# Kernel tuning notes

Hardware: AMD Instinct MI355X
Metric: run time of the kernel (lower is better)

Reference implementation:

```python
import jax, jax.numpy as jnp
import numpy as np

H = 8   # num_heads
K = 7   # kernel_size


def setup_inputs() -> dict:
    key = jax.random.key(0)
    k1, k2, k3 = jax.random.split(key, 3)
    T, B, C = 2048, 16, 512
    x = jax.random.normal(k1, (T, B, C), dtype=jnp.float32)
    query = jax.random.normal(k2, (T, B, C), dtype=jnp.float32)
    W = jax.random.normal(k3, (C, H * K), dtype=jnp.float32) * 0.02
    return {"x": x, "query": query, "W": W}


def reference(x, query, W):
    T, B, C = x.shape
    R = C // H
    # per-position, per-head kernel weights: Dense(H*K) on query, no bias
    weight = jnp.einsum('tbc,cn->tbn', query, W).reshape(T * B * H, K)
    weight = jax.nn.softmax(weight, axis=-1)  # weight_softmax=True; dropout rate 0 is identity
    # TF extract_patches with SAME padding along T: total pad K-1, more on the bottom
    pad_before = (K - 1) // 2
    pad_after = K - 1 - pad_before
    x_pad = jnp.pad(x, ((pad_before, pad_after), (0, 0), (0, 0)))
    idx = jnp.arange(T)[:, None] + jnp.arange(K)[None, :]  # (T, K)
    patches = x_pad[idx]                      # (T, K, B, C)
    patches = jnp.transpose(patches, (0, 2, 1, 3))  # (T, B, K, C): TF depth order is (k, c)
    # Faithful to the source: flat (K*C) axis reinterpreted as (H, R, K)
    x_unfold = patches.reshape(T * B * H, R, K)
    out = jnp.einsum('nrk,nk->nr', x_unfold, weight)  # batched tiny matmul
    return out.reshape(T, B, C)
```

## Files before the change

### kernel.cpp

```cpp
#include <hip/hip_runtime.h>

#define T_DIM 2048
#define B_DIM 16
#define C_DIM 512
#define NW 56
#define XS_BYTES (22 * 512 * 2)
#define A_OFF    XS_BYTES
#define WT_OFF   (XS_BYTES + 4160)
#define LDS_TOTAL (XS_BYTES + 16384)

typedef __attribute__((ext_vector_type(8))) short short8;
typedef __attribute__((ext_vector_type(4))) float floatx4;

static __device__ __forceinline__ unsigned short f2bf(float x) {
    union { float f; unsigned u; } v; v.f = x;
    return (unsigned short)((v.u + 0x7FFFu + ((v.u >> 16) & 1u)) >> 16);
}
static __device__ __forceinline__ float bf_lo(unsigned u) {
    union { unsigned u; float f; } c; c.u = u << 16; return c.f;
}
static __device__ __forceinline__ float bf_hi(unsigned u) {
    union { unsigned u; float f; } c; c.u = u & 0xFFFF0000u; return c.f;
}
static __device__ __forceinline__ int swz(int a) { return a ^ ((a >> 3) & 0x70); }

__global__ __launch_bounds__(256)
void pack_w(const float* __restrict__ W, short8* __restrict__ Bg) {
    const int g  = blockIdx.x * 256 + threadIdx.x;
    const int ks = g >> 8;
    const int nt = (g >> 6) & 3;
    const int l  = g & 63;
    const int n  = nt * 16 + (l & 15);
    const int k0 = ks * 32 + ((l >> 4) & 3) * 8;
    short8 o;
#pragma unroll
    for (int j = 0; j < 8; ++j) {
        const float v = (n < NW) ? W[(size_t)(k0 + j) * NW + n] : 0.f;
        o[j] = (short)f2bf(v);
    }
    Bg[g] = o;
}

__global__ __launch_bounds__(256)
void fused_kernel(const float* __restrict__ x, const float* __restrict__ q,
                  const short8* __restrict__ Bg, float* __restrict__ out) {
    __shared__ __align__(16) char S[LDS_TOTAL];

    const int tid  = threadIdx.x;
    const int lane = tid & 63;
    const int wv   = tid >> 6;
    const int b    = blockIdx.x & 15;
    const int t0   = (blockIdx.x >> 4) * 16;

    const int rq = lane & 15;
    const int qq = lane >> 4;
    const float* qrow = q + ((size_t)(t0 + rq) * B_DIM + b) * C_DIM + qq * 8;
    float4 qr[4][2];
#pragma unroll
    for (int s = 0; s < 4; ++s) {
        const int ks = wv + s * 4;
        qr[s][0] = *(const float4*)(qrow + ks * 32);
        qr[s][1] = *(const float4*)(qrow + ks * 32 + 4);
    }
    short8 bfr[16];
#pragma unroll
    for (int ks = 0; ks < 16; ++ks)
        bfr[ks] = Bg[(ks * 4 + wv) * 64 + lane];
    float4 xr[11];
#pragma unroll
    for (int j = 0; j < 11; ++j) {
        const int idx = tid + j * 256;
        const int i   = idx >> 7;
        const int c   = (idx & 127) * 4;
        const int tp  = t0 + i - 3;
        xr[j] = make_float4(0.f, 0.f, 0.f, 0.f);
        if (tp >= 0 && tp < T_DIM)
            xr[j] = *(const float4*)(x + ((size_t)tp * B_DIM + b) * C_DIM + c);
    }

    short8* A8 = (short8*)(S + A_OFF);
#pragma unroll
    for (int s = 0; s < 4; ++s) {
        const int ks = wv + s * 4;
        short8 o;
        o[0] = (short)f2bf(qr[s][0].x); o[1] = (short)f2bf(qr[s][0].y);
        o[2] = (short)f2bf(qr[s][0].z); o[3] = (short)f2bf(qr[s][0].w);
        o[4] = (short)f2bf(qr[s][1].x); o[5] = (short)f2bf(qr[s][1].y);
        o[6] = (short)f2bf(qr[s][1].z); o[7] = (short)f2bf(qr[s][1].w);
        A8[ks * 64 + lane] = o;
    }
    __syncthreads();

    floatx4 acc = (floatx4){0.f, 0.f, 0.f, 0.f};
#pragma unroll
    for (int ks = 0; ks < 16; ++ks) {
        const short8 af = A8[ks * 64 + lane];
        acc = __builtin_amdgcn_mfma_f32_16x16x32_bf16(af, bfr[ks], acc, 0, 0, 0);
    }

    char* XS = S;
#pragma unroll
    for (int j = 0; j < 11; ++j) {
        const int idx = tid + j * 256;
        uint2 p;
        p.x = (unsigned)f2bf(xr[j].x) | ((unsigned)f2bf(xr[j].y) << 16);
        p.y = (unsigned)f2bf(xr[j].z) | ((unsigned)f2bf(xr[j].w) << 16);
        const int a = idx * 8;
        *(uint2*)(XS + swz(a)) = p;
    }
    __syncthreads();

    float* L = (float*)(S + A_OFF);
    const int m = lane & 15;
    const int quad = lane >> 4;
#pragma unroll
    for (int r = 0; r < 4; ++r)
        L[(quad * 4 + r) * 65 + wv * 16 + m] = acc[r];
    __syncthreads();

    float* wt = (float*)(S + WT_OFF);
    if (tid < 128) {
        const int row = tid >> 3, h = tid & 7;
        const float* Lp = L + row * 65 + h * 7;
        float mx = Lp[0];
#pragma unroll
        for (int k = 1; k < 7; ++k) mx = fmaxf(mx, Lp[k]);
        float e[7], sm = 0.f;
#pragma unroll
        for (int k = 0; k < 7; ++k) { e[k] = __expf(Lp[k] - mx); sm += e[k]; }
        const float inv = 1.0f / sm;
#pragma unroll
        for (int k = 0; k < 7; ++k) wt[row * NW + h * 7 + k] = e[k] * inv;
    }
    __syncthreads();

    const int h = lane >> 3;
    const int base_b = lane * 112;
#pragma unroll
    for (int s = 0; s < 4; ++s) {
        const int tt = wv * 4 + s;
        const int tb = tt * 1024 + base_b;
        uint4 xu[7];
#pragma unroll
        for (int i = 0; i < 7; ++i)
            xu[i] = *(const uint4*)(XS + swz(tb + i * 16));
        float xf[56];
#pragma unroll
        for (int i = 0; i < 7; ++i) {
            xf[i * 8 + 0] = bf_lo(xu[i].x); xf[i * 8 + 1] = bf_hi(xu[i].x);
            xf[i * 8 + 2] = bf_lo(xu[i].y); xf[i * 8 + 3] = bf_hi(xu[i].y);
            xf[i * 8 + 4] = bf_lo(xu[i].z); xf[i * 8 + 5] = bf_hi(xu[i].z);
            xf[i * 8 + 6] = bf_lo(xu[i].w); xf[i * 8 + 7] = bf_hi(xu[i].w);
        }
        const float* wp = wt + tt * NW + h * 7;
        float w[7];
#pragma unroll
        for (int k = 0; k < 7; ++k) w[k] = wp[k];
        float a8[8];
#pragma unroll
        for (int r = 0; r < 8; ++r) {
            float sacc = xf[r * 7] * w[0];
#pragma unroll
            for (int k = 1; k < 7; ++k) sacc = fmaf(w[k], xf[r * 7 + k], sacc);
            a8[r] = sacc;
        }
        float* orow = out + ((size_t)(t0 + tt) * B_DIM + b) * C_DIM + lane * 8;
        *(float4*)(orow)     = make_float4(a8[0], a8[1], a8[2], a8[3]);
        *(float4*)(orow + 4) = make_float4(a8[4], a8[5], a8[6], a8[7]);
    }
}

extern "C" void kernel_launch(void* const* d_in, const int* in_sizes, int n_in,
                              void* d_out, int out_size, void* d_ws, size_t ws_size,
                              hipStream_t stream) {
    const float* x = (const float*)d_in[0];
    const float* q = (const float*)d_in[1];
    const float* W = (const float*)d_in[2];
    float* out = (float*)d_out;
    short8* Bg = (short8*)d_ws;

    pack_w<<<16, 256, 0, stream>>>(W, Bg);
    fused_kernel<<<(T_DIM / 16) * B_DIM, 256, 0, stream>>>(x, q, Bg, out);
}
```

Baseline: 174.2 us.

## Split fused kernel into weight and conv kernels with global softmax weights

Splits the fused kernel in two. One kernel computes the projection GEMM and softmax and writes per-position weights to workspace. A second conv kernel with lower LDS use and a launch-bounds occupancy hint reads x and those weights and uses nontemporal stores for the output. The aim is to lower register and LDS pressure so more blocks fit per CU, at the cost of an extra launch and a global round trip for about 7 MB of weights. The old fused path is kept as a fallback when the workspace is too small.

```diff
diff --git a/kernel.cpp b/kernel.cpp
--- a/kernel.cpp
+++ b/kernel.cpp
@@ -4,10 +4,17 @@
 #define B_DIM 16
 #define C_DIM 512
 #define NW 56
+
 #define XS_BYTES (22 * 512 * 2)
 #define A_OFF    XS_BYTES
 #define WT_OFF   (XS_BYTES + 4160)
 #define LDS_TOTAL (XS_BYTES + 16384)
+
+#define W_L_OFF   16384
+#define W_WT_OFF  (16384 + 4160)
+#define W_LDS     (16384 + 4160 + 3584)
+#define C_WT_OFF  XS_BYTES
+#define C_LDS     (XS_BYTES + 3584)
 
 typedef __attribute__((ext_vector_type(8))) short short8;
 typedef __attribute__((ext_vector_type(4))) float floatx4;
@@ -42,9 +49,9 @@
 }
 
 __global__ __launch_bounds__(256)
-void fused_kernel(const float* __restrict__ x, const float* __restrict__ q,
-                  const short8* __restrict__ Bg, float* __restrict__ out) {
-    __shared__ __align__(16) char S[LDS_TOTAL];
+void weight_kernel(const float* __restrict__ q, const short8* __restrict__ Bg,
+                   float* __restrict__ wt_g) {
+    __shared__ __align__(16) char S[W_LDS];
 
     const int tid  = threadIdx.x;
     const int lane = tid & 63;
@@ -66,6 +73,70 @@
 #pragma unroll
     for (int ks = 0; ks < 16; ++ks)
         bfr[ks] = Bg[(ks * 4 + wv) * 64 + lane];
+
+    short8* A8 = (short8*)S;
+#pragma unroll
+    for (int s = 0; s < 4; ++s) {
+        const int ks = wv + s * 4;
+        short8 o;
+        o[0] = (short)f2bf(qr[s][0].x); o[1] = (short)f2bf(qr[s][0].y);
+        o[2] = (short)f2bf(qr[s][0].z); o[3] = (short)f2bf(qr[s][0].w);
+        o[4] = (short)f2bf(qr[s][1].x); o[5] = (short)f2bf(qr[s][1].y);
+        o[6] = (short)f2bf(qr[s][1].z); o[7] = (short)f2bf(qr[s][1].w);
+        A8[ks * 64 + lane] = o;
+    }
+    __syncthreads();
+
+    floatx4 acc = (floatx4){0.f, 0.f, 0.f, 0.f};
+#pragma unroll
+    for (int ks = 0; ks < 16; ++ks) {
+        const short8 af = A8[ks * 64 + lane];
+        acc = __builtin_amdgcn_mfma_f32_16x16x32_bf16(af, bfr[ks], acc, 0, 0, 0);
+    }
+
+    float* L = (float*)(S + W_L_OFF);
+    const int m = lane & 15;
+    const int quad = lane >> 4;
+#pragma unroll
+    for (int r = 0; r < 4; ++r)
+        L[(quad * 4 + r) * 65 + wv * 16 + m] = acc[r];
+    __syncthreads();
+
+    float* wt = (float*)(S + W_WT_OFF);
+    if (tid < 128) {
+        const int row = tid >> 3, h = tid & 7;
+        const float* Lp = L + row * 65 + h * 7;
+        float mx = Lp[0];
+#pragma unroll
+        for (int k = 1; k < 7; ++k) mx = fmaxf(mx, Lp[k]);
+        float e[7], sm = 0.f;
+#pragma unroll
+        for (int k = 0; k < 7; ++k) { e[k] = __expf(Lp[k] - mx); sm += e[k]; }
+        const float inv = 1.0f / sm;
+#pragma unroll
+        for (int k = 0; k < 7; ++k) wt[row * NW + h * 7 + k] = e[k] * inv;
+    }
+    __syncthreads();
+
+    if (tid < 224) {
+        const int row = tid / 14;
+        const int j   = tid - row * 14;
+        const float4 v = *(const float4*)(wt + row * NW + j * 4);
+        *(float4*)(wt_g + ((size_t)(t0 + row) * B_DIM + b) * NW + j * 4) = v;
+    }
+}
+
+__global__ __launch_bounds__(256, 6)
+void conv_kernel(const float* __restrict__ x, const float* __restrict__ wt_g,
+                 float* __restrict__ out) {
+    __shared__ __align__(16) char S[C_LDS];
+
+    const int tid  = threadIdx.x;
+    const int lane = tid & 63;
+    const int wv   = tid >> 6;
+    const int b    = blockIdx.x & 15;
+    const int t0   = (blockIdx.x >> 4) * 16;
+
     float4 xr[11];
 #pragma unroll
     for (int j = 0; j < 11; ++j) {
@@ -77,26 +148,11 @@
         if (tp >= 0 && tp < T_DIM)
             xr[j] = *(const float4*)(x + ((size_t)tp * B_DIM + b) * C_DIM + c);
     }
-
-    short8* A8 = (short8*)(S + A_OFF);
-#pragma unroll
-    for (int s = 0; s < 4; ++s) {
-        const int ks = wv + s * 4;
-        short8 o;
-        o[0] = (short)f2bf(qr[s][0].x); o[1] = (short)f2bf(qr[s][0].y);
-        o[2] = (short)f2bf(qr[s][0].z); o[3] = (short)f2bf(qr[s][0].w);
-        o[4] = (short)f2bf(qr[s][1].x); o[5] = (short)f2bf(qr[s][1].y);
-        o[6] = (short)f2bf(qr[s][1].z); o[7] = (short)f2bf(qr[s][1].w);
-        A8[ks * 64 + lane] = o;
-    }
-    __syncthreads();
-
-    floatx4 acc = (floatx4){0.f, 0.f, 0.f, 0.f};
-#pragma unroll
-    for (int ks = 0; ks < 16; ++ks) {
-        const short8 af = A8[ks * 64 + lane];
-        acc = __builtin_amdgcn_mfma_f32_16x16x32_bf16(af, bfr[ks], acc, 0, 0, 0);
-    }
+    const int row = tid / 14;
+    const int jw  = tid - row * 14;
+    float4 wld = make_float4(0.f, 0.f, 0.f, 0.f);
+    if (tid < 224)
+        wld = *(const float4*)(wt_g + ((size_t)(t0 + row) * B_DIM + b) * NW + jw * 4);
 
     char* XS = S;
 #pragma unroll
@@ -105,35 +161,13 @@
         uint2 p;
         p.x = (unsigned)f2bf(xr[j].x) | ((unsigned)f2bf(xr[j].y) << 16);
         p.y = (unsigned)f2bf(xr[j].z) | ((unsigned)f2bf(xr[j].w) << 16);
-        const int a = idx * 8;
-        *(uint2*)(XS + swz(a)) = p;
-    }
-    __syncthreads();
-
-    float* L = (float*)(S + A_OFF);
-    const int m = lane & 15;
-    const int quad = lane >> 4;
-#pragma unroll
-    for (int r = 0; r < 4; ++r)
-        L[(quad * 4 + r) * 65 + wv * 16 + m] = acc[r];
-    __syncthreads();
-
-    float* wt = (float*)(S + WT_OFF);
-    if (tid < 128) {
-        const int row = tid >> 3, h = tid & 7;
-        const float* Lp = L + row * 65 + h * 7;
-        float mx = Lp[0];
-#pragma unroll
-        for (int k = 1; k < 7; ++k) mx = fmaxf(mx, Lp[k]);
-        float e[7], sm = 0.f;
-#pragma unroll
-        for (int k = 0; k < 7; ++k) { e[k] = __expf(Lp[k] - mx); sm += e[k]; }
-        const float inv = 1.0f / sm;
-#pragma unroll
-        for (int k = 0; k < 7; ++k) wt[row * NW + h * 7 + k] = e[k] * inv;
-    }
-    __syncthreads();
-
+        *(uint2*)(XS + swz(idx * 8)) = p;
+    }
+    if (tid < 224)
+        *(float4*)(S + C_WT_OFF + (row * NW + jw * 4) * 4) = wld;
+    __syncthreads();
+
+    const float* wt = (const float*)(S + C_WT_OFF);
     const int h = lane >> 3;
     const int base_b = lane * 112;
 #pragma unroll
@@ -165,6 +199,137 @@
             a8[r] = sacc;
         }
         float* orow = out + ((size_t)(t0 + tt) * B_DIM + b) * C_DIM + lane * 8;
+        floatx4 v0 = (floatx4){a8[0], a8[1], a8[2], a8[3]};
+        floatx4 v1 = (floatx4){a8[4], a8[5], a8[6], a8[7]};
+        __builtin_nontemporal_store(v0, (floatx4*)orow);
+        __builtin_nontemporal_store(v1, (floatx4*)(orow + 4));
+    }
+}
+
+__global__ __launch_bounds__(256)
+void fused_kernel(const float* __restrict__ x, const float* __restrict__ q,
+                  const short8* __restrict__ Bg, float* __restrict__ out) {
+    __shared__ __align__(16) char S[LDS_TOTAL];
+
+    const int tid  = threadIdx.x;
+    const int lane = tid & 63;
+    const int wv   = tid >> 6;
+    const int b    = blockIdx.x & 15;
+    const int t0   = (blockIdx.x >> 4) * 16;
+
+    const int rq = lane & 15;
+    const int qq = lane >> 4;
+    const float* qrow = q + ((size_t)(t0 + rq) * B_DIM + b) * C_DIM + qq * 8;
+    float4 qr[4][2];
+#pragma unroll
+    for (int s = 0; s < 4; ++s) {
+        const int ks = wv + s * 4;
+        qr[s][0] = *(const float4*)(qrow + ks * 32);
+        qr[s][1] = *(const float4*)(qrow + ks * 32 + 4);
+    }
+    short8 bfr[16];
+#pragma unroll
+    for (int ks = 0; ks < 16; ++ks)
+        bfr[ks] = Bg[(ks * 4 + wv) * 64 + lane];
+    float4 xr[11];
+#pragma unroll
+    for (int j = 0; j < 11; ++j) {
+        const int idx = tid + j * 256;
+        const int i   = idx >> 7;
+        const int c   = (idx & 127) * 4;
+        const int tp  = t0 + i - 3;
+        xr[j] = make_float4(0.f, 0.f, 0.f, 0.f);
+        if (tp >= 0 && tp < T_DIM)
+            xr[j] = *(const float4*)(x + ((size_t)tp * B_DIM + b) * C_DIM + c);
+    }
+
+    short8* A8 = (short8*)(S + A_OFF);
+#pragma unroll
+    for (int s = 0; s < 4; ++s) {
+        const int ks = wv + s * 4;
+        short8 o;
+        o[0] = (short)f2bf(qr[s][0].x); o[1] = (short)f2bf(qr[s][0].y);
+        o[2] = (short)f2bf(qr[s][0].z); o[3] = (short)f2bf(qr[s][0].w);
+        o[4] = (short)f2bf(qr[s][1].x); o[5] = (short)f2bf(qr[s][1].y);
+        o[6] = (short)f2bf(qr[s][1].z); o[7] = (short)f2bf(qr[s][1].w);
+        A8[ks * 64 + lane] = o;
+    }
+    __syncthreads();
+
+    floatx4 acc = (floatx4){0.f, 0.f, 0.f, 0.f};
+#pragma unroll
+    for (int ks = 0; ks < 16; ++ks) {
+        const short8 af = A8[ks * 64 + lane];
+        acc = __builtin_amdgcn_mfma_f32_16x16x32_bf16(af, bfr[ks], acc, 0, 0, 0);
+    }
+
+    char* XS = S;
+#pragma unroll
+    for (int j = 0; j < 11; ++j) {
+        const int idx = tid + j * 256;
+        uint2 p;
+        p.x = (unsigned)f2bf(xr[j].x) | ((unsigned)f2bf(xr[j].y) << 16);
+        p.y = (unsigned)f2bf(xr[j].z) | ((unsigned)f2bf(xr[j].w) << 16);
+        const int a = idx * 8;
+        *(uint2*)(XS + swz(a)) = p;
+    }
+    __syncthreads();
+
+    float* L = (float*)(S + A_OFF);
+    const int m = lane & 15;
+    const int quad = lane >> 4;
+#pragma unroll
+    for (int r = 0; r < 4; ++r)
+        L[(quad * 4 + r) * 65 + wv * 16 + m] = acc[r];
+    __syncthreads();
+
+    float* wt = (float*)(S + WT_OFF);
+    if (tid < 128) {
+        const int row = tid >> 3, h = tid & 7;
+        const float* Lp = L + row * 65 + h * 7;
+        float mx = Lp[0];
+#pragma unroll
+        for (int k = 1; k < 7; ++k) mx = fmaxf(mx, Lp[k]);
+        float e[7], sm = 0.f;
+#pragma unroll
+        for (int k = 0; k < 7; ++k) { e[k] = __expf(Lp[k] - mx); sm += e[k]; }
+        const float inv = 1.0f / sm;
+#pragma unroll
+        for (int k = 0; k < 7; ++k) wt[row * NW + h * 7 + k] = e[k] * inv;
+    }
+    __syncthreads();
+
+    const int h = lane >> 3;
+    const int base_b = lane * 112;
+#pragma unroll
+    for (int s = 0; s < 4; ++s) {
+        const int tt = wv * 4 + s;
+        const int tb = tt * 1024 + base_b;
+        uint4 xu[7];
+#pragma unroll
+        for (int i = 0; i < 7; ++i)
+            xu[i] = *(const uint4*)(XS + swz(tb + i * 16));
+        float xf[56];
+#pragma unroll
+        for (int i = 0; i < 7; ++i) {
+            xf[i * 8 + 0] = bf_lo(xu[i].x); xf[i * 8 + 1] = bf_hi(xu[i].x);
+            xf[i * 8 + 2] = bf_lo(xu[i].y); xf[i * 8 + 3] = bf_hi(xu[i].y);
+            xf[i * 8 + 4] = bf_lo(xu[i].z); xf[i * 8 + 5] = bf_hi(xu[i].z);
+            xf[i * 8 + 6] = bf_lo(xu[i].w); xf[i * 8 + 7] = bf_hi(xu[i].w);
+        }
+        const float* wp = wt + tt * NW + h * 7;
+        float w[7];
+#pragma unroll
+        for (int k = 0; k < 7; ++k) w[k] = wp[k];
+        float a8[8];
+#pragma unroll
+        for (int r = 0; r < 8; ++r) {
+            float sacc = xf[r * 7] * w[0];
+#pragma unroll
+            for (int k = 1; k < 7; ++k) sacc = fmaf(w[k], xf[r * 7 + k], sacc);
+            a8[r] = sacc;
+        }
+        float* orow = out + ((size_t)(t0 + tt) * B_DIM + b) * C_DIM + lane * 8;
         *(float4*)(orow)     = make_float4(a8[0], a8[1], a8[2], a8[3]);
         *(float4*)(orow + 4) = make_float4(a8[4], a8[5], a8[6], a8[7]);
     }
@@ -180,5 +345,13 @@
     short8* Bg = (short8*)d_ws;
 
     pack_w<<<16, 256, 0, stream>>>(W, Bg);
-    fused_kernel<<<(T_DIM / 16) * B_DIM, 256, 0, stream>>>(x, q, Bg, out);
-}
+
+    const size_t wt_bytes = (size_t)T_DIM * B_DIM * NW * sizeof(float);
+    if (ws_size >= 65536 + wt_bytes) {
+        float* wt_g = (float*)((char*)d_ws + 65536);
+        weight_kernel<<<(T_DIM / 16) * B_DIM, 256, 0, stream>>>(q, Bg, wt_g);
+        conv_kernel<<<(T_DIM / 16) * B_DIM, 256, 0, stream>>>(x, wt_g, out);
+    } else {
+        fused_kernel<<<(T_DIM / 16) * B_DIM, 256, 0, stream>>>(x, q, Bg, out);
+    }
+}
```

After: 182.9 us. 1.05x slower.

## Repack weight columns per head and compute softmax in-register via wave shuffles

Applied to the files above, without the earlier changes.

Weight columns are repacked so each wave's 16-column MFMA tile holds two whole heads (14 valid columns). This lets the softmax run inside the wave with shuffles instead of staging logits through LDS behind extra barriers. The q tile now streams straight from global into the MFMA loop, skipping the LDS A-staging, and the x loads move after the GEMM, which shrinks LDS use and register pressure and may raise occupancy. Outputs use nontemporal stores. In exchange, x global latency is no longer hidden behind the GEMM, and each column lane does redundant shuffles and exps.

```diff
diff --git a/kernel.cpp b/kernel.cpp
--- a/kernel.cpp
+++ b/kernel.cpp
@@ -4,10 +4,10 @@
 #define B_DIM 16
 #define C_DIM 512
 #define NW 56
+
 #define XS_BYTES (22 * 512 * 2)
-#define A_OFF    XS_BYTES
-#define WT_OFF   (XS_BYTES + 4160)
-#define LDS_TOTAL (XS_BYTES + 16384)
+#define WT_OFF   XS_BYTES
+#define F_LDS    (XS_BYTES + 3584)
 
 typedef __attribute__((ext_vector_type(8))) short short8;
 typedef __attribute__((ext_vector_type(4))) float floatx4;
@@ -30,21 +30,22 @@
     const int ks = g >> 8;
     const int nt = (g >> 6) & 3;
     const int l  = g & 63;
-    const int n  = nt * 16 + (l & 15);
+    const int c  = l & 15;
+    const int n  = nt * 14 + c;
     const int k0 = ks * 32 + ((l >> 4) & 3) * 8;
     short8 o;
 #pragma unroll
     for (int j = 0; j < 8; ++j) {
-        const float v = (n < NW) ? W[(size_t)(k0 + j) * NW + n] : 0.f;
+        const float v = (c < 14) ? W[(size_t)(k0 + j) * NW + n] : 0.f;
         o[j] = (short)f2bf(v);
     }
     Bg[g] = o;
 }
 
 __global__ __launch_bounds__(256)
-void fused_kernel(const float* __restrict__ x, const float* __restrict__ q,
-                  const short8* __restrict__ Bg, float* __restrict__ out) {
-    __shared__ __align__(16) char S[LDS_TOTAL];
+void fused1(const float* __restrict__ x, const float* __restrict__ q,
+            const short8* __restrict__ Bg, float* __restrict__ out) {
+    __shared__ __align__(16) char S[F_LDS];
 
     const int tid  = threadIdx.x;
     const int lane = tid & 63;
@@ -54,84 +55,64 @@
 
     const int rq = lane & 15;
     const int qq = lane >> 4;
-    const float* qrow = q + ((size_t)(t0 + rq) * B_DIM + b) * C_DIM + qq * 8;
-    float4 qr[4][2];
-#pragma unroll
-    for (int s = 0; s < 4; ++s) {
-        const int ks = wv + s * 4;
-        qr[s][0] = *(const float4*)(qrow + ks * 32);
-        qr[s][1] = *(const float4*)(qrow + ks * 32 + 4);
-    }
-    short8 bfr[16];
-#pragma unroll
-    for (int ks = 0; ks < 16; ++ks)
-        bfr[ks] = Bg[(ks * 4 + wv) * 64 + lane];
-    float4 xr[11];
-#pragma unroll
-    for (int j = 0; j < 11; ++j) {
-        const int idx = tid + j * 256;
-        const int i   = idx >> 7;
-        const int c   = (idx & 127) * 4;
-        const int tp  = t0 + i - 3;
-        xr[j] = make_float4(0.f, 0.f, 0.f, 0.f);
-        if (tp >= 0 && tp < T_DIM)
-            xr[j] = *(const float4*)(x + ((size_t)tp * B_DIM + b) * C_DIM + c);
+    const float* qbase = q + ((size_t)(t0 + rq) * B_DIM + b) * C_DIM + qq * 8;
+    floatx4 acc = (floatx4){0.f, 0.f, 0.f, 0.f};
+#pragma unroll 4
+    for (int ks = 0; ks < 16; ++ks) {
+        const float4 f0 = *(const float4*)(qbase + ks * 32);
+        const float4 f1 = *(const float4*)(qbase + ks * 32 + 4);
+        const short8 bf = Bg[(ks * 4 + wv) * 64 + lane];
+        short8 af;
+        af[0] = (short)f2bf(f0.x); af[1] = (short)f2bf(f0.y);
+        af[2] = (short)f2bf(f0.z); af[3] = (short)f2bf(f0.w);
+        af[4] = (short)f2bf(f1.x); af[5] = (short)f2bf(f1.y);
+        af[6] = (short)f2bf(f1.z); af[7] = (short)f2bf(f1.w);
+        acc = __builtin_amdgcn_mfma_f32_16x16x32_bf16(af, bf, acc, 0, 0, 0);
     }
 
-    short8* A8 = (short8*)(S + A_OFF);
+    const int c    = lane & 15;
+    const int cb   = (c < 7) ? 0 : 7;
+    const int sb   = (lane & 48) + cb;
+    const int quad = lane >> 4;
+    float* wt = (float*)(S + WT_OFF);
 #pragma unroll
-    for (int s = 0; s < 4; ++s) {
-        const int ks = wv + s * 4;
-        short8 o;
-        o[0] = (short)f2bf(qr[s][0].x); o[1] = (short)f2bf(qr[s][0].y);
-        o[2] = (short)f2bf(qr[s][0].z); o[3] = (short)f2bf(qr[s][0].w);
-        o[4] = (short)f2bf(qr[s][1].x); o[5] = (short)f2bf(qr[s][1].y);
-        o[6] = (short)f2bf(qr[s][1].z); o[7] = (short)f2bf(qr[s][1].w);
-        A8[ks * 64 + lane] = o;
+    for (int r = 0; r < 4; ++r) {
+        const float a = acc[r];
+        const float v0 = __shfl(a, sb + 0);
+        const float v1 = __shfl(a, sb + 1);
+        const float v2 = __shfl(a, sb + 2);
+        const float v3 = __shfl(a, sb + 3);
+        const float v4 = __shfl(a, sb + 4);
+        const float v5 = __shfl(a, sb + 5);
+        const float v6 = __shfl(a, sb + 6);
+        const float mx = fmaxf(fmaxf(fmaxf(v0, v1), fmaxf(v2, v3)),
+                               fmaxf(fmaxf(v4, v5), v6));
+        const float sm = __expf(v0 - mx) + __expf(v1 - mx) + __expf(v2 - mx) +
+                         __expf(v3 - mx) + __expf(v4 - mx) + __expf(v5 - mx) +
+                         __expf(v6 - mx);
+        const float w = __expf(a - mx) * (1.0f / sm);
+        if (c < 14)
+            wt[(quad * 4 + r) * NW + wv * 14 + c] = w;
     }
-    __syncthreads();
 
-    floatx4 acc = (floatx4){0.f, 0.f, 0.f, 0.f};
-#pragma unroll
-    for (int ks = 0; ks < 16; ++ks) {
-        const short8 af = A8[ks * 64 + lane];
-        acc = __builtin_amdgcn_mfma_f32_16x16x32_bf16(af, bfr[ks], acc, 0, 0, 0);
-    }
+    __builtin_amdgcn_sched_barrier(0);
 
     char* XS = S;
 #pragma unroll
     for (int j = 0; j < 11; ++j) {
         const int idx = tid + j * 256;
+        const int i   = idx >> 7;
+        const int cc  = (idx & 127) * 4;
+        const int tp  = t0 + i - 3;
+        float4 xv = make_float4(0.f, 0.f, 0.f, 0.f);
+        if (tp >= 0 && tp < T_DIM)
+            xv = *(const float4*)(x + ((size_t)tp * B_DIM + b) * C_DIM + cc);
         uint2 p;
-        p.x = (unsigned)f2bf(xr[j].x) | ((unsigned)f2bf(xr[j].y) << 16);
-        p.y = (unsigned)f2bf(xr[j].z) | ((unsigned)f2bf(xr[j].w) << 16);
-        const int a = idx * 8;
-        *(uint2*)(XS + swz(a)) = p;
+        p.x = (unsigned)f2bf(xv.x) | ((unsigned)f2bf(xv.y) << 16);
+        p.y = (unsigned)f2bf(xv.z) | ((unsigned)f2bf(xv.w) << 16);
+        *(uint2*)(XS + swz(idx * 8)) = p;
     }
-    __syncthreads();
 
-    float* L = (float*)(S + A_OFF);
-    const int m = lane & 15;
-    const int quad = lane >> 4;
-#pragma unroll
-    for (int r = 0; r < 4; ++r)
-        L[(quad * 4 + r) * 65 + wv * 16 + m] = acc[r];
-    __syncthreads();
-
-    float* wt = (float*)(S + WT_OFF);
-    if (tid < 128) {
-        const int row = tid >> 3, h = tid & 7;
-        const float* Lp = L + row * 65 + h * 7;
-        float mx = Lp[0];
-#pragma unroll
-        for (int k = 1; k < 7; ++k) mx = fmaxf(mx, Lp[k]);
-        float e[7], sm = 0.f;
-#pragma unroll
-        for (int k = 0; k < 7; ++k) { e[k] = __expf(Lp[k] - mx); sm += e[k]; }
-        const float inv = 1.0f / sm;
-#pragma unroll
-        for (int k = 0; k < 7; ++k) wt[row * NW + h * 7 + k] = e[k] * inv;
-    }
     __syncthreads();
 
     const int h = lane >> 3;
@@ -165,8 +146,10 @@
             a8[r] = sacc;
         }
         float* orow = out + ((size_t)(t0 + tt) * B_DIM + b) * C_DIM + lane * 8;
-        *(float4*)(orow)     = make_float4(a8[0], a8[1], a8[2], a8[3]);
-        *(float4*)(orow + 4) = make_float4(a8[4], a8[5], a8[6], a8[7]);
+        floatx4 v0 = (floatx4){a8[0], a8[1], a8[2], a8[3]};
+        floatx4 v1 = (floatx4){a8[4], a8[5], a8[6], a8[7]};
+        __builtin_nontemporal_store(v0, (floatx4*)orow);
+        __builtin_nontemporal_store(v1, (floatx4*)(orow + 4));
     }
 }
 
@@ -180,5 +163,5 @@
     short8* Bg = (short8*)d_ws;
 
     pack_w<<<16, 256, 0, stream>>>(W, Bg);
-    fused_kernel<<<(T_DIM / 16) * B_DIM, 256, 0, stream>>>(x, q, Bg, out);
+    fused1<<<(T_DIM / 16) * B_DIM, 256, 0, stream>>>(x, q, Bg, out);
 }
```

Measured after the change: 201.2 us. 15.5% more time.
